# Performance work log

Measured on AMD Instinct MI355X. Metric: run time of the kernel, lower is better.

Reference implementation:

```python
import jax, jax.numpy as jnp
import numpy as np

N_NODES = 20000
N_EDGES = 320000
IN_DIM = 256
OUT_DIM = 256
H1, H2 = 640, 320


def _linear_params(key, fan_in, fan_out):
    k1, k2 = jax.random.split(key)
    bound = 1.0 / np.sqrt(fan_in)
    w = jax.random.uniform(k1, (fan_in, fan_out), minval=-bound, maxval=bound, dtype=jnp.float32)
    b = jax.random.uniform(k2, (fan_out,), minval=-bound, maxval=bound, dtype=jnp.float32)
    return w, b


def setup_inputs() -> dict:
    key = jax.random.key(0)
    ks = jax.random.split(key, 10)
    features = jax.random.normal(ks[0], (N_NODES, IN_DIM), dtype=jnp.float32)
    edge_index = jax.random.randint(ks[1], (2, N_EDGES), 0, N_NODES, dtype=jnp.int64)
    w1a, b1a = _linear_params(ks[2], IN_DIM, H1)
    w1b, b1b = _linear_params(ks[3], H1, H1)
    w2a, b2a = _linear_params(ks[4], H1, H2)
    w2b, b2b = _linear_params(ks[5], H2, H2)
    w3a, b3a = _linear_params(ks[6], H2, OUT_DIM)
    w3b, b3b = _linear_params(ks[7], OUT_DIM, OUT_DIM)
    wr, br = _linear_params(ks[8], IN_DIM, OUT_DIM)
    return dict(features=features, edge_index=edge_index,
                w1a=w1a, b1a=b1a, w1b=w1b, b1b=b1b,
                w2a=w2a, b2a=b2a, w2b=w2b, b2b=b2b,
                w3a=w3a, b3a=b3a, w3b=w3b, b3b=b3b,
                wr=wr, br=br)


def _gin_layer(x, src, dst, wa, ba, wb, bb):
    # DGL GINConv 'sum': h = (1+eps)*x + sum_{src->dst} x[src], eps=0
    agg = jax.ops.segment_sum(x[src], dst, num_segments=N_NODES)
    h = x + agg
    h = jax.nn.elu(h @ wa + ba)
    h = jax.nn.elu(h @ wb + bb)
    return h


def reference(features, edge_index, w1a, b1a, w1b, b1b, w2a, b2a, w2b, b2b,
              w3a, b3a, w3b, b3b, wr, br):
    src, dst = edge_index[0], edge_index[1]
    res = jax.nn.elu(features @ wr + br)
    x = jax.nn.elu(_gin_layer(features, src, dst, w1a, b1a, w1b, b1b))
    # dropout (p=0.2) omitted: eval mode
    x = jax.nn.elu(_gin_layer(x, src, dst, w2a, b2a, w2b, b2b))
    x = _gin_layer(x, src, dst, w3a, b3a, w3b, b3b)
    return (x, res)
```

## Files before the change

### kernel.cpp

```cpp
#include <hip/hip_runtime.h>
#include <cstdint>
#include <cstddef>

#define NN 20000
#define NE 320000

typedef short short8 __attribute__((ext_vector_type(8)));
typedef float f32x4 __attribute__((ext_vector_type(4)));
typedef unsigned short u16;

__device__ __forceinline__ float b2f(u16 u) {
  union { unsigned int i; float f; } z; z.i = ((unsigned int)u) << 16; return z.f;
}
__device__ __forceinline__ u16 f2b(float f) {
  union { float f; unsigned int i; } z; z.f = f;
  unsigned int r = z.i + 0x7fffu + ((z.i >> 16) & 1u);
  return (u16)(r >> 16);
}
__device__ __forceinline__ float eluf(float v) {
  return v > 0.0f ? v : __expf(v) - 1.0f;
}

__global__ __launch_bounds__(256) void k_prep(
    const float* __restrict__ features, u16* __restrict__ xbf,
    const float* __restrict__ wr, const float* __restrict__ w1a,
    const float* __restrict__ w1b, const float* __restrict__ w2a,
    const float* __restrict__ w2b, const float* __restrict__ w3a,
    const float* __restrict__ w3b,
    u16* __restrict__ wrt, u16* __restrict__ w1at, u16* __restrict__ w1bt,
    u16* __restrict__ w2at, u16* __restrict__ w2bt, u16* __restrict__ w3at,
    u16* __restrict__ w3bt) {
  int tid = blockIdx.x * 256 + threadIdx.x;
  if (tid < 1280000) {
    int i = tid * 4;
    float4 v = *reinterpret_cast<const float4*>(features + i);
    ushort4 o;
    o.x = f2b(v.x); o.y = f2b(v.y); o.z = f2b(v.z); o.w = f2b(v.w);
    *reinterpret_cast<ushort4*>(xbf + i) = o;
    return;
  }
  int r = tid - 1280000;
  const float* Ws[7] = {wr, w1a, w1b, w2a, w2b, w3a, w3b};
  u16* Wts[7] = {wrt, w1at, w1bt, w2at, w2bt, w3at, w3bt};
  const int Kd[7] = {256, 256, 640, 640, 320, 320, 256};
  const int Nd[7] = {256, 640, 640, 320, 320, 256, 256};
  const int cnt[7] = {65536, 163840, 409600, 204800, 102400, 81920, 65536};
#pragma unroll
  for (int j = 0; j < 7; ++j) {
    if (r < cnt[j]) {
      int n = r / Kd[j], k = r - n * Kd[j];
      Wts[j][r] = f2b(Ws[j][(size_t)k * Nd[j] + n]);
      return;
    }
    r -= cnt[j];
  }
}

__global__ __launch_bounds__(256) void k_hist(const int* __restrict__ dst,
                                              int* __restrict__ counts, int ne) {
  int i = blockIdx.x * 256 + threadIdx.x;
  if (i < ne) atomicAdd(&counts[dst[i]], 1);
}

__global__ __launch_bounds__(1024) void k_scan(const int* __restrict__ counts,
                                               int* __restrict__ rs,
                                               int* __restrict__ cur) {
  __shared__ int wsum[16];
  __shared__ int carry_s;
  int t = threadIdx.x;
  int l = t & 63, w = t >> 6;
  if (t == 0) carry_s = 0;
  __syncthreads();
  for (int base = 0; base < NN; base += 4096) {
    int idx = base + t * 4;
    int4 v = {0, 0, 0, 0};
    if (idx < NN) v = *reinterpret_cast<const int4*>(counts + idx);
    int p0 = v.x, p1 = p0 + v.y, p2 = p1 + v.z, p3 = p2 + v.w;
    int incl = p3;
#pragma unroll
    for (int off = 1; off < 64; off <<= 1) {
      int u = __shfl_up(incl, off, 64);
      if (l >= off) incl += u;
    }
    if (l == 63) wsum[w] = incl;
    __syncthreads();
    int carry = carry_s;
    int wpre = 0;
    for (int k2 = 0; k2 < w; ++k2) wpre += wsum[k2];
    int tot = 0;
    if (t == 0)
      for (int k2 = 0; k2 < 16; ++k2) tot += wsum[k2];
    int ex = carry + wpre + incl - p3;
    if (idx < NN) {
      int4 o;
      o.x = ex; o.y = ex + p0; o.z = ex + p1; o.w = ex + p2;
      *reinterpret_cast<int4*>(rs + idx) = o;
      *reinterpret_cast<int4*>(cur + idx) = o;
    }
    __syncthreads();
    if (t == 0) carry_s = carry + tot;
    __syncthreads();
  }
  if (t == 0) rs[NN] = carry_s;
}

__global__ __launch_bounds__(256) void k_scatter(const int* __restrict__ src,
                                                 const int* __restrict__ dst,
                                                 int* __restrict__ cursor,
                                                 int* __restrict__ csr_src, int ne) {
  int i = blockIdx.x * 256 + threadIdx.x;
  if (i >= ne) return;
  int d = dst[i];
  int p = atomicAdd(&cursor[d], 1);
  csr_src[p] = src[i];
}

template <int D, int ACT>
__global__ __launch_bounds__(256) void k_agg(const u16* __restrict__ x,
                                             const int* __restrict__ rs,
                                             const int* __restrict__ cs,
                                             const float* __restrict__ bias,
                                             u16* __restrict__ h) {
  constexpr int NC = D / 8;
  int tid = blockIdx.x * 256 + threadIdx.x;
  if (tid >= NN * NC) return;
  int node = tid / NC;
  int c = tid - node * NC;
  const u16* xp = x + (size_t)c * 8;
  float acc[8];
  {
    short8 v = *reinterpret_cast<const short8*>(xp + (size_t)node * D);
#pragma unroll
    for (int q = 0; q < 8; ++q) acc[q] = b2f((u16)v[q]);
  }
  int e0 = rs[node], e1 = rs[node + 1];
  int e = e0;
  for (; e + 8 <= e1; e += 8) {
    int s[8];
#pragma unroll
    for (int u = 0; u < 8; ++u) s[u] = cs[e + u];
    short8 v[8];
#pragma unroll
    for (int u = 0; u < 8; ++u)
      v[u] = *reinterpret_cast<const short8*>(xp + (size_t)s[u] * D);
#pragma unroll
    for (int q = 0; q < 8; ++q) {
      float a0 = b2f((u16)v[0][q]) + b2f((u16)v[1][q]);
      float a1 = b2f((u16)v[2][q]) + b2f((u16)v[3][q]);
      float a2 = b2f((u16)v[4][q]) + b2f((u16)v[5][q]);
      float a3 = b2f((u16)v[6][q]) + b2f((u16)v[7][q]);
      acc[q] += (a0 + a1) + (a2 + a3);
    }
  }
  for (; e + 4 <= e1; e += 4) {
    int s0 = cs[e], s1 = cs[e + 1], s2 = cs[e + 2], s3 = cs[e + 3];
    short8 v0 = *reinterpret_cast<const short8*>(xp + (size_t)s0 * D);
    short8 v1 = *reinterpret_cast<const short8*>(xp + (size_t)s1 * D);
    short8 v2 = *reinterpret_cast<const short8*>(xp + (size_t)s2 * D);
    short8 v3 = *reinterpret_cast<const short8*>(xp + (size_t)s3 * D);
#pragma unroll
    for (int q = 0; q < 8; ++q)
      acc[q] += (b2f((u16)v0[q]) + b2f((u16)v1[q])) + (b2f((u16)v2[q]) + b2f((u16)v3[q]));
  }
  for (; e < e1; ++e) {
    int s = cs[e];
    short8 v = *reinterpret_cast<const short8*>(xp + (size_t)s * D);
#pragma unroll
    for (int q = 0; q < 8; ++q) acc[q] += b2f((u16)v[q]);
  }
  if (ACT == 1) {
    float4 b0 = *reinterpret_cast<const float4*>(bias + c * 8);
    float4 b1 = *reinterpret_cast<const float4*>(bias + c * 8 + 4);
    acc[0] = eluf(acc[0] + b0.x); acc[1] = eluf(acc[1] + b0.y);
    acc[2] = eluf(acc[2] + b0.z); acc[3] = eluf(acc[3] + b0.w);
    acc[4] = eluf(acc[4] + b1.x); acc[5] = eluf(acc[5] + b1.y);
    acc[6] = eluf(acc[6] + b1.z); acc[7] = eluf(acc[7] + b1.w);
  }
  short8 o;
#pragma unroll
  for (int q = 0; q < 8; ++q) o[q] = (short)f2b(acc[q]);
  *reinterpret_cast<short8*>(h + (size_t)node * D + (size_t)c * 8) = o;
}

template <int BM, int K, int N, int ACT, bool OUTF32>
__global__ __launch_bounds__(256) void k_gemm(const u16* __restrict__ A,
                                              const u16* __restrict__ Bt,
                                              const float* __restrict__ bias,
                                              void* __restrict__ outp, int M) {
  constexpr int NBY = (N + 127) / 128;
  constexpr int NK = K / 32;
  constexpr int ABUF = BM * 32;
  constexpr int BUFSZ = ABUF + 4096;
  constexpr int MI = BM / 32;
  constexpr int LPT = BM / 64 + 2;
  __shared__ __align__(16) u16 smem[3 * BUFSZ];
  int t = threadIdx.x;
  int l = t & 63, w = t >> 6;
  int lm = l & 15, lk = l >> 4;

  int nb = gridDim.x;
  int q8 = nb >> 3, r8 = nb & 7;
  int orig = blockIdx.x;
  int xcd = orig & 7, idx = orig >> 3;
  int wg = (xcd < r8 ? xcd * (q8 + 1) : r8 * (q8 + 1) + (xcd - r8) * q8) + idx;
  int m0 = (wg / NBY) * BM;
  int n0 = (wg % NBY) * 128;
  int wm = (w >> 1) * (BM / 2), wn = (w & 1) * 64;

  f32x4 acc[MI][4];
#pragma unroll
  for (int i = 0; i < MI; ++i)
#pragma unroll
    for (int j = 0; j < 4; ++j)
#pragma unroll
      for (int qq = 0; qq < 4; ++qq) acc[i][j][qq] = 0.0f;

  auto stage = [&](int buf, int kt) {
    int k0 = kt * 32;
    u16* As = smem + buf * BUFSZ;
    u16* Bs = As + ABUF;
#pragma unroll
    for (int it = 0; it < BM / 64; ++it) {
      int c = it * 256 + t;
      int row = c >> 2;
      int kc = (c & 3) ^ ((c >> 3) & 3);
      int ra = m0 + row; ra = ra < M ? ra : M - 1;
      const u16* ga = A + (size_t)ra * K + k0 + kc * 8;
      __builtin_amdgcn_global_load_lds(
          (const __attribute__((address_space(1))) void*)ga,
          (__attribute__((address_space(3))) void*)(As + c * 8), 16, 0, 0);
    }
#pragma unroll
    for (int it = 0; it < 2; ++it) {
      int c = it * 256 + t;
      int row = c >> 2;
      int kc = (c & 3) ^ ((c >> 3) & 3);
      int rb = n0 + row; rb = rb < N ? rb : N - 1;
      const u16* gb = Bt + (size_t)rb * K + k0 + kc * 8;
      __builtin_amdgcn_global_load_lds(
          (const __attribute__((address_space(1))) void*)gb,
          (__attribute__((address_space(3))) void*)(Bs + c * 8), 16, 0, 0);
    }
  };

  int kidx = (lk ^ ((lm >> 1) & 3)) * 8;

  stage(0, 0);
  stage(1, 1);
  stage(2, 2);
  int buf = 0;
  for (int kt = 0; kt < NK; ++kt) {
    int rem = NK - 1 - kt;
    if (rem >= 2)
      asm volatile("s_waitcnt vmcnt(%0)" ::"n"(2 * LPT) : "memory");
    else if (rem == 1)
      asm volatile("s_waitcnt vmcnt(%0)" ::"n"(LPT) : "memory");
    else
      asm volatile("s_waitcnt vmcnt(0)" ::: "memory");
    __builtin_amdgcn_s_barrier();
    asm volatile("" ::: "memory");
    const u16* As = smem + buf * BUFSZ;
    const u16* Bs = As + ABUF;
    short8 af[MI], bf[4];
#pragma unroll
    for (int i = 0; i < MI; ++i)
      af[i] = *reinterpret_cast<const short8*>(As + (wm + i * 16 + lm) * 32 + kidx);
#pragma unroll
    for (int j = 0; j < 4; ++j)
      bf[j] = *reinterpret_cast<const short8*>(Bs + (wn + j * 16 + lm) * 32 + kidx);
    __builtin_amdgcn_s_setprio(1);
#pragma unroll
    for (int i = 0; i < MI; ++i)
#pragma unroll
      for (int j = 0; j < 4; ++j)
        acc[i][j] = __builtin_amdgcn_mfma_f32_16x16x32_bf16(af[i], bf[j], acc[i][j], 0, 0, 0);
    __builtin_amdgcn_s_setprio(0);
    asm volatile("s_waitcnt lgkmcnt(0)" ::: "memory");
    __builtin_amdgcn_s_barrier();
    asm volatile("" ::: "memory");
    if (kt + 3 < NK) stage(buf, kt + 3);
    buf = (buf == 2) ? 0 : buf + 1;
  }

  if (!OUTF32) {
    u16* ep = smem + w * (BM / 2) * 64;
#pragma unroll
    for (int j = 0; j < 4; ++j) {
      int col = n0 + wn + j * 16 + lm;
      float bv = (ACT > 0) ? bias[col < N ? col : N - 1] : 0.0f;
#pragma unroll
      for (int i = 0; i < MI; ++i)
#pragma unroll
        for (int qq = 0; qq < 4; ++qq) {
          float v = acc[i][j][qq];
          if (ACT > 0) { v += bv; v = eluf(v); }
          if (ACT == 2) v = eluf(v);
          ep[(i * 16 + lk * 4 + qq) * 64 + j * 16 + lm] = f2b(v);
        }
    }
    __syncthreads();
    u16* op = (u16*)outp;
#pragma unroll
    for (int u = 0; u < BM / 16; ++u) {
      int rrow = m0 + wm + u * 8 + (l >> 3);
      int col = n0 + wn + (l & 7) * 8;
      if (rrow < M && col < N)
        *reinterpret_cast<short8*>(op + (size_t)rrow * N + col) =
            *reinterpret_cast<const short8*>(ep + u * 512 + l * 8);
    }
  } else {
    float* op = (float*)outp;
#pragma unroll
    for (int j = 0; j < 4; ++j) {
      int col = n0 + wn + j * 16 + lm;
      if (col >= N) continue;
      float bv = (ACT > 0) ? bias[col] : 0.0f;
#pragma unroll
      for (int i = 0; i < MI; ++i) {
        int rb = m0 + wm + i * 16 + lk * 4;
#pragma unroll
        for (int qq = 0; qq < 4; ++qq) {
          int rr = rb + qq;
          if (rr >= M) continue;
          float v = acc[i][j][qq];
          if (ACT > 0) { v += bv; v = eluf(v); }
          if (ACT == 2) v = eluf(v);
          op[(size_t)rr * N + col] = v;
        }
      }
    }
  }
}

extern "C" void kernel_launch(void* const* d_in, const int* in_sizes, int n_in,
                              void* d_out, int out_size, void* d_ws, size_t ws_size,
                              hipStream_t stream) {
  const float* features = (const float*)d_in[0];
  const int* eidx = (const int*)d_in[1];
  const float* w1a = (const float*)d_in[2];
  const float* b1a = (const float*)d_in[3];
  const float* w1b = (const float*)d_in[4];
  const float* b1b = (const float*)d_in[5];
  const float* w2a = (const float*)d_in[6];
  const float* b2a = (const float*)d_in[7];
  const float* w2b = (const float*)d_in[8];
  const float* b2b = (const float*)d_in[9];
  const float* w3a = (const float*)d_in[10];
  const float* b3a = (const float*)d_in[11];
  const float* w3b = (const float*)d_in[12];
  const float* b3b = (const float*)d_in[13];
  const float* wr = (const float*)d_in[14];
  const float* br = (const float*)d_in[15];

  char* ws = (char*)d_ws;
  u16* bufA = (u16*)(ws);
  u16* bufB = (u16*)(ws + 25600000);
  u16* wrt = (u16*)(ws + 51200000);
  u16* w1at = wrt + 256 * 256;
  u16* w1bt = w1at + 640 * 256;
  u16* w2at = w1bt + 640 * 640;
  u16* w2bt = w2at + 320 * 640;
  u16* w3at = w2bt + 320 * 320;
  u16* w3bt = w3at + 256 * 320;
  int* row_start = (int*)(ws + 53387264);
  int* cursor = row_start + 20004;
  int* csr_src = cursor + NN;
  int* counts = csr_src + NE;

  const int* esrc = eidx;
  const int* edst = eidx + NE;

  hipMemsetAsync(counts, 0, NN * sizeof(int), stream);
  k_hist<<<(NE + 255) / 256, 256, 0, stream>>>(edst, counts, NE);
  k_scan<<<1, 1024, 0, stream>>>(counts, row_start, cursor);
  k_scatter<<<(NE + 255) / 256, 256, 0, stream>>>(esrc, edst, cursor, csr_src, NE);

  k_prep<<<9272, 256, 0, stream>>>(features, bufA, wr, w1a, w1b, w2a, w2b, w3a,
                                   w3b, wrt, w1at, w1bt, w2at, w2bt, w3at, w3bt);

  float* out_x = (float*)d_out;
  float* out_res = (float*)d_out + (size_t)NN * 256;

  k_gemm<64, 256, 256, 1, true><<<dim3(313 * 2), 256, 0, stream>>>(bufA, wrt, br, out_res, NN);
  k_agg<256, 0><<<2500, 256, 0, stream>>>(bufA, row_start, csr_src, nullptr, bufB);
  k_gemm<64, 256, 640, 1, false><<<dim3(313 * 5), 256, 0, stream>>>(bufB, w1at, b1a, bufA, NN);
  k_gemm<64, 640, 640, 2, false><<<dim3(313 * 5), 256, 0, stream>>>(bufA, w1bt, b1b, bufB, NN);
  k_gemm<64, 640, 320, 0, false><<<dim3(313 * 3), 256, 0, stream>>>(bufB, w2at, nullptr, bufA, NN);
  k_agg<320, 1><<<3125, 256, 0, stream>>>(bufA, row_start, csr_src, b2a, bufB);
  k_gemm<64, 320, 320, 2, false><<<dim3(313 * 3), 256, 0, stream>>>(bufB, w2bt, b2b, bufA, NN);
  k_gemm<64, 320, 256, 0, false><<<dim3(313 * 2), 256, 0, stream>>>(bufA, w3at, nullptr, bufB, NN);
  k_agg<256, 1><<<2500, 256, 0, stream>>>(bufB, row_start, csr_src, b3a, bufA);
  k_gemm<64, 256, 256, 1, true><<<dim3(313 * 2), 256, 0, stream>>>(bufA, w3bt, b3b, out_x, NN);
}
```

Measured before the change: 269.4 us.

## Store aggregation inputs in column-sliced layout and fold histogram into prep kernel

The bf16 feature matrix and the outputs of the GEMMs that feed aggregation are now written in four column slices, each stored contiguously per node. The aggregation kernel assigns each block one slice and half the nodes, so the gathered working set per slice is a quarter as large and should fit better in L2/MALL during random neighbor gathers. The edge-degree histogram is merged into the prep kernel to remove one launch. The cost is extra index arithmetic, narrower 128/160-byte rows per gather, and a GEMM A-load path that has to read the sliced layout.

```diff
diff --git a/kernel.cpp b/kernel.cpp
--- a/kernel.cpp
+++ b/kernel.cpp
@@ -22,7 +22,8 @@
 }
 
 __global__ __launch_bounds__(256) void k_prep(
-    const float* __restrict__ features, u16* __restrict__ xbf,
+    const float* __restrict__ features, u16* __restrict__ xbf_sliced,
+    const int* __restrict__ edst, int* __restrict__ counts,
     const float* __restrict__ wr, const float* __restrict__ w1a,
     const float* __restrict__ w1b, const float* __restrict__ w2a,
     const float* __restrict__ w2b, const float* __restrict__ w3a,
@@ -32,14 +33,21 @@
     u16* __restrict__ w3bt) {
   int tid = blockIdx.x * 256 + threadIdx.x;
   if (tid < 1280000) {
-    int i = tid * 4;
-    float4 v = *reinterpret_cast<const float4*>(features + i);
+    int node = tid >> 6;
+    int c4 = (tid & 63) * 4;
+    float4 v = *reinterpret_cast<const float4*>(features + (size_t)node * 256 + c4);
     ushort4 o;
     o.x = f2b(v.x); o.y = f2b(v.y); o.z = f2b(v.z); o.w = f2b(v.w);
-    *reinterpret_cast<ushort4*>(xbf + i) = o;
+    int slice = c4 >> 6, within = c4 & 63;
+    *reinterpret_cast<ushort4*>(xbf_sliced + (size_t)slice * NN * 64 +
+                                (size_t)node * 64 + within) = o;
     return;
   }
-  int r = tid - 1280000;
+  if (tid < 1600000) {
+    atomicAdd(&counts[edst[tid - 1280000]], 1);
+    return;
+  }
+  int r = tid - 1600000;
   const float* Ws[7] = {wr, w1a, w1b, w2a, w2b, w3a, w3b};
   u16* Wts[7] = {wrt, w1at, w1bt, w2at, w2bt, w3at, w3bt};
   const int Kd[7] = {256, 256, 640, 640, 320, 320, 256};
@@ -54,12 +62,6 @@
     }
     r -= cnt[j];
   }
-}
-
-__global__ __launch_bounds__(256) void k_hist(const int* __restrict__ dst,
-                                              int* __restrict__ counts, int ne) {
-  int i = blockIdx.x * 256 + threadIdx.x;
-  if (i < ne) atomicAdd(&counts[dst[i]], 1);
 }
 
 __global__ __launch_bounds__(1024) void k_scan(const int* __restrict__ counts,
@@ -116,20 +118,27 @@
 }
 
 template <int D, int ACT>
-__global__ __launch_bounds__(256) void k_agg(const u16* __restrict__ x,
+__global__ __launch_bounds__(256) void k_agg(const u16* __restrict__ xs,
                                              const int* __restrict__ rs,
                                              const int* __restrict__ cs,
                                              const float* __restrict__ bias,
                                              u16* __restrict__ h) {
-  constexpr int NC = D / 8;
-  int tid = blockIdx.x * 256 + threadIdx.x;
-  if (tid >= NN * NC) return;
-  int node = tid / NC;
-  int c = tid - node * NC;
-  const u16* xp = x + (size_t)c * 8;
+  constexpr int SW = D / 4;
+  constexpr int NCs = SW / 8;
+  constexpr int NPB = 256 / NCs;
+  int b = blockIdx.x;
+  int cls = b & 7;
+  int slice = cls & 3;
+  int half = cls >> 2;
+  int t = threadIdx.x;
+  int nl = t / NCs, ch = t - nl * NCs;
+  if (nl >= NPB) return;
+  int node = half * 10000 + (b >> 3) * NPB + nl;
+  if (node >= (half ? NN : 10000)) return;
+  const u16* xp = xs + (size_t)slice * NN * SW + (size_t)ch * 8;
   float acc[8];
   {
-    short8 v = *reinterpret_cast<const short8*>(xp + (size_t)node * D);
+    short8 v = *reinterpret_cast<const short8*>(xp + (size_t)node * SW);
 #pragma unroll
     for (int q = 0; q < 8; ++q) acc[q] = b2f((u16)v[q]);
   }
@@ -142,7 +151,7 @@
     short8 v[8];
 #pragma unroll
     for (int u = 0; u < 8; ++u)
-      v[u] = *reinterpret_cast<const short8*>(xp + (size_t)s[u] * D);
+      v[u] = *reinterpret_cast<const short8*>(xp + (size_t)s[u] * SW);
 #pragma unroll
     for (int q = 0; q < 8; ++q) {
       float a0 = b2f((u16)v[0][q]) + b2f((u16)v[1][q]);
@@ -154,23 +163,24 @@
   }
   for (; e + 4 <= e1; e += 4) {
     int s0 = cs[e], s1 = cs[e + 1], s2 = cs[e + 2], s3 = cs[e + 3];
-    short8 v0 = *reinterpret_cast<const short8*>(xp + (size_t)s0 * D);
-    short8 v1 = *reinterpret_cast<const short8*>(xp + (size_t)s1 * D);
-    short8 v2 = *reinterpret_cast<const short8*>(xp + (size_t)s2 * D);
-    short8 v3 = *reinterpret_cast<const short8*>(xp + (size_t)s3 * D);
+    short8 v0 = *reinterpret_cast<const short8*>(xp + (size_t)s0 * SW);
+    short8 v1 = *reinterpret_cast<const short8*>(xp + (size_t)s1 * SW);
+    short8 v2 = *reinterpret_cast<const short8*>(xp + (size_t)s2 * SW);
+    short8 v3 = *reinterpret_cast<const short8*>(xp + (size_t)s3 * SW);
 #pragma unroll
     for (int q = 0; q < 8; ++q)
       acc[q] += (b2f((u16)v0[q]) + b2f((u16)v1[q])) + (b2f((u16)v2[q]) + b2f((u16)v3[q]));
   }
   for (; e < e1; ++e) {
     int s = cs[e];
-    short8 v = *reinterpret_cast<const short8*>(xp + (size_t)s * D);
+    short8 v = *reinterpret_cast<const short8*>(xp + (size_t)s * SW);
 #pragma unroll
     for (int q = 0; q < 8; ++q) acc[q] += b2f((u16)v[q]);
   }
+  int col0 = slice * SW + ch * 8;
   if (ACT == 1) {
-    float4 b0 = *reinterpret_cast<const float4*>(bias + c * 8);
-    float4 b1 = *reinterpret_cast<const float4*>(bias + c * 8 + 4);
+    float4 b0 = *reinterpret_cast<const float4*>(bias + col0);
+    float4 b1 = *reinterpret_cast<const float4*>(bias + col0 + 4);
     acc[0] = eluf(acc[0] + b0.x); acc[1] = eluf(acc[1] + b0.y);
     acc[2] = eluf(acc[2] + b0.z); acc[3] = eluf(acc[3] + b0.w);
     acc[4] = eluf(acc[4] + b1.x); acc[5] = eluf(acc[5] + b1.y);
@@ -179,10 +189,10 @@
   short8 o;
 #pragma unroll
   for (int q = 0; q < 8; ++q) o[q] = (short)f2b(acc[q]);
-  *reinterpret_cast<short8*>(h + (size_t)node * D + (size_t)c * 8) = o;
-}
-
-template <int BM, int K, int N, int ACT, bool OUTF32>
+  *reinterpret_cast<short8*>(h + (size_t)node * D + col0) = o;
+}
+
+template <int BM, int K, int N, int ACT, bool OUTF32, bool INS, int OSW>
 __global__ __launch_bounds__(256) void k_gemm(const u16* __restrict__ A,
                                               const u16* __restrict__ Bt,
                                               const float* __restrict__ bias,
@@ -225,7 +235,11 @@
       int row = c >> 2;
       int kc = (c & 3) ^ ((c >> 3) & 3);
       int ra = m0 + row; ra = ra < M ? ra : M - 1;
-      const u16* ga = A + (size_t)ra * K + k0 + kc * 8;
+      const u16* ga;
+      if (INS)
+        ga = A + (size_t)(k0 >> 6) * NN * 64 + (size_t)ra * 64 + (k0 & 63) + kc * 8;
+      else
+        ga = A + (size_t)ra * K + k0 + kc * 8;
       __builtin_amdgcn_global_load_lds(
           (const __attribute__((address_space(1))) void*)ga,
           (__attribute__((address_space(3))) void*)(As + c * 8), 16, 0, 0);
@@ -304,9 +318,16 @@
     for (int u = 0; u < BM / 16; ++u) {
       int rrow = m0 + wm + u * 8 + (l >> 3);
       int col = n0 + wn + (l & 7) * 8;
-      if (rrow < M && col < N)
-        *reinterpret_cast<short8*>(op + (size_t)rrow * N + col) =
-            *reinterpret_cast<const short8*>(ep + u * 512 + l * 8);
+      if (rrow < M && col < N) {
+        short8 val = *reinterpret_cast<const short8*>(ep + u * 512 + l * 8);
+        if (OSW) {
+          int slice = col / OSW, within = col - slice * OSW;
+          *reinterpret_cast<short8*>(op + (size_t)slice * NN * OSW +
+                                     (size_t)rrow * OSW + within) = val;
+        } else {
+          *reinterpret_cast<short8*>(op + (size_t)rrow * N + col) = val;
+        }
+      }
     }
   } else {
     float* op = (float*)outp;
@@ -371,24 +392,23 @@
   const int* edst = eidx + NE;
 
   hipMemsetAsync(counts, 0, NN * sizeof(int), stream);
-  k_hist<<<(NE + 255) / 256, 256, 0, stream>>>(edst, counts, NE);
+  k_prep<<<10523, 256, 0, stream>>>(features, bufA, edst, counts, wr, w1a, w1b,
+                                    w2a, w2b, w3a, w3b, wrt, w1at, w1bt, w2at,
+                                    w2bt, w3at, w3bt);
   k_scan<<<1, 1024, 0, stream>>>(counts, row_start, cursor);
   k_scatter<<<(NE + 255) / 256, 256, 0, stream>>>(esrc, edst, cursor, csr_src, NE);
 
-  k_prep<<<9272, 256, 0, stream>>>(features, bufA, wr, w1a, w1b, w2a, w2b, w3a,
-                                   w3b, wrt, w1at, w1bt, w2at, w2bt, w3at, w3bt);
-
   float* out_x = (float*)d_out;
   float* out_res = (float*)d_out + (size_t)NN * 256;
 
-  k_gemm<64, 256, 256, 1, true><<<dim3(313 * 2), 256, 0, stream>>>(bufA, wrt, br, out_res, NN);
-  k_agg<256, 0><<<2500, 256, 0, stream>>>(bufA, row_start, csr_src, nullptr, bufB);
-  k_gemm<64, 256, 640, 1, false><<<dim3(313 * 5), 256, 0, stream>>>(bufB, w1at, b1a, bufA, NN);
-  k_gemm<64, 640, 640, 2, false><<<dim3(313 * 5), 256, 0, stream>>>(bufA, w1bt, b1b, bufB, NN);
-  k_gemm<64, 640, 320, 0, false><<<dim3(313 * 3), 256, 0, stream>>>(bufB, w2at, nullptr, bufA, NN);
-  k_agg<320, 1><<<3125, 256, 0, stream>>>(bufA, row_start, csr_src, b2a, bufB);
-  k_gemm<64, 320, 320, 2, false><<<dim3(313 * 3), 256, 0, stream>>>(bufB, w2bt, b2b, bufA, NN);
-  k_gemm<64, 320, 256, 0, false><<<dim3(313 * 2), 256, 0, stream>>>(bufA, w3at, nullptr, bufB, NN);
-  k_agg<256, 1><<<2500, 256, 0, stream>>>(bufB, row_start, csr_src, b3a, bufA);
-  k_gemm<64, 256, 256, 1, true><<<dim3(313 * 2), 256, 0, stream>>>(bufA, w3bt, b3b, out_x, NN);
-}
+  k_gemm<64, 256, 256, 1, true, true, 0><<<dim3(313 * 2), 256, 0, stream>>>(bufA, wrt, br, out_res, NN);
+  k_agg<256, 0><<<8 * 313, 256, 0, stream>>>(bufA, row_start, csr_src, nullptr, bufB);
+  k_gemm<64, 256, 640, 1, false, false, 0><<<dim3(313 * 5), 256, 0, stream>>>(bufB, w1at, b1a, bufA, NN);
+  k_gemm<64, 640, 640, 2, false, false, 0><<<dim3(313 * 5), 256, 0, stream>>>(bufA, w1bt, b1b, bufB, NN);
+  k_gemm<64, 640, 320, 0, false, false, 80><<<dim3(313 * 3), 256, 0, stream>>>(bufB, w2at, nullptr, bufA, NN);
+  k_agg<320, 1><<<8 * 400, 256, 0, stream>>>(bufA, row_start, csr_src, b2a, bufB);
+  k_gemm<64, 320, 320, 2, false, false, 0><<<dim3(313 * 3), 256, 0, stream>>>(bufB, w2bt, b2b, bufA, NN);
+  k_gemm<64, 320, 256, 0, false, false, 64><<<dim3(313 * 2), 256, 0, stream>>>(bufA, w3at, nullptr, bufB, NN);
+  k_agg<256, 1><<<8 * 313, 256, 0, stream>>>(bufB, row_start, csr_src, b3a, bufA);
+  k_gemm<64, 256, 256, 1, true, false, 0><<<dim3(313 * 2), 256, 0, stream>>>(bufA, w3bt, b3b, out_x, NN);
+}
```

After: 257.7 us. 4.3% less time.
